# Kernel optimization log

Measured on AMD Instinct MI355X. Metric: run time of the kernel, lower is better.

The kernel has to match this reference:

```python
import jax, jax.numpy as jnp
import numpy as np
from jax import lax

EPS = 1e-4       # BatchNorm eps from module
THRESHOLD = 0.0  # TernaryActive threshold (default)

B, C_IN, H, W = 16, 32, 256, 256
C_OUT, K, STRIDE, PAD = 32, 3, 1, 1


def setup_inputs() -> dict:
    key = jax.random.key(0)
    ks = jax.random.split(key, 7)
    x = jax.random.normal(ks[0], (B, C_IN, H, W), dtype=jnp.float32)
    bn_gamma = jax.random.normal(ks[1], (C_IN,), dtype=jnp.float32) * 0.1 + 1.0
    bn_beta = jax.random.normal(ks[2], (C_IN,), dtype=jnp.float32) * 0.1
    bn_mean = jax.random.normal(ks[3], (C_IN,), dtype=jnp.float32) * 0.1
    bn_var = jax.random.uniform(ks[4], (C_IN,), dtype=jnp.float32, minval=0.5, maxval=1.5)
    fan_in = C_IN * K * K
    bound = 1.0 / np.sqrt(fan_in)
    conv_w = jax.random.uniform(ks[5], (C_OUT, C_IN, K, K), dtype=jnp.float32, minval=-bound, maxval=bound)
    conv_b = jax.random.uniform(ks[6], (C_OUT,), dtype=jnp.float32, minval=-bound, maxval=bound)
    return {"x": x, "bn_gamma": bn_gamma, "bn_beta": bn_beta,
            "bn_mean": bn_mean, "bn_var": bn_var,
            "conv_w": conv_w, "conv_b": conv_b}


def _ternary(x):
    # torch: output[x >= thr] = 1, then output[x <= -thr] = -1 (le overrides ge)
    return jnp.where(x <= -THRESHOLD, -1.0,
                     jnp.where(x >= THRESHOLD, 1.0, 0.0)).astype(x.dtype)


def reference(x, bn_gamma, bn_beta, bn_mean, bn_var, conv_w, conv_b):
    # BatchNorm2d (inference form with running stats), per-channel over C
    inv = bn_gamma / jnp.sqrt(bn_var + EPS)
    xh = x * inv[None, :, None, None] + (bn_beta - bn_mean * inv)[None, :, None, None]
    # Ternary quantize {-1, 0, 1}
    q = _ternary(xh)
    # Conv2d 3x3, stride 1, pad 1 (NCHW / OIHW)
    y = lax.conv_general_dilated(q, conv_w, window_strides=(STRIDE, STRIDE),
                                 padding=[(PAD, PAD), (PAD, PAD)],
                                 dimension_numbers=("NCHW", "OIHW", "NCHW"))
    y = y + conv_b[None, :, None, None]
    # ReLU
    return jnp.maximum(y, 0.0)
```

## Files before the change

kernel.cpp:

```cpp
#include <hip/hip_runtime.h>


#define B_    16
#define H_    256
#define W_    256
#define SW    32
#define YC    32
#define ROWB  2304
#define NITEM 576

typedef __bf16 bf16x8 __attribute__((ext_vector_type(8)));
typedef float  f32x4  __attribute__((ext_vector_type(4)));
union FragCast { int4 i; bf16x8 b; };

__device__ __forceinline__ unsigned short f2bf(float f) {
    union { float f; unsigned u; } c; c.f = f;
    unsigned u = c.u;
    u += 0x7FFFu + ((u >> 16) & 1u);
    return (unsigned short)(u >> 16);
}

__device__ __forceinline__ unsigned short quant1(float v, float sc, float sh) {
    float xh = __fadd_rn(__fmul_rn(v, sc), sh);
    return (xh <= 0.0f) ? (unsigned short)0xBF80u
         : ((xh >= 0.0f) ? (unsigned short)0x3F80u : (unsigned short)0u);
}

__launch_bounds__(256, 4)
__global__ void tbconv_kernel(const float* __restrict__ x,
                              const float* __restrict__ bn_g,
                              const float* __restrict__ bn_b,
                              const float* __restrict__ bn_m,
                              const float* __restrict__ bn_v,
                              const float* __restrict__ conv_w,
                              const float* __restrict__ conv_b,
                              float* __restrict__ out)
{
    __shared__ __align__(16) unsigned char smem[18432];
    __shared__ float sScale[32], sShift[32];
    unsigned int*  sW = (unsigned int*)smem;
    unsigned char* sQ = smem;

    const int tid = threadIdx.x;
    const int bx  = blockIdx.x;
    const int strip = bx >> 7;
    const int b     = (bx >> 3) & 15;
    const int yc    = bx & 7;
    const int x0 = strip * SW;
    const int y0 = yc * YC;

    if (tid < 32) {
        float s = __fdiv_rn(bn_g[tid], __fsqrt_rn(__fadd_rn(bn_v[tid], 1e-4f)));
        sScale[tid] = s;
        sShift[tid] = __fsub_rn(bn_b[tid], __fmul_rn(bn_m[tid], s));
    }
    for (int j = tid; j < 4608; j += 256) {
        int cp = j & 15, co = (j >> 4) & 31, t = j >> 9;
        float w0 = conv_w[(co * 32 + 2 * cp)     * 9 + t];
        float w1 = conv_w[(co * 32 + 2 * cp + 1) * 9 + t];
        sW[j] = (unsigned)f2bf(w0) | ((unsigned)f2bf(w1) << 16);
    }
    __syncthreads();

    const float* lp[3];
    int   lw0[3], lw1[3];
    float lsc[3], lsh[3];
    bool  lxok[3];
    const bool lv2 = (tid < 64);
    #pragma unroll
    for (int j = 0; j < 3; ++j) {
        int i = tid + 256 * j; if (i >= NITEM) i = 0;
        int ci = i / 18, pr = i - 18 * ci;
        int gx = x0 - 2 + 2 * pr;
        bool xok = (gx >= 0) && (gx < W_);
        int gxc = (gx < 0) ? 0 : ((gx > 254) ? 254 : gx);
        lp[j]   = x + (((size_t)(b * 32 + ci)) << 16) + gxc;
        lxok[j] = xok;
        int hx0 = 2 * pr - 1, hx1 = 2 * pr;
        int hc0 = (hx0 < 0)  ? 34 : hx0;
        int hc1 = (hx1 > 33) ? 35 : hx1;
        int q = ci >> 3, cl = ci & 7;
        lw0[j] = ((hc0 * 4 + (q ^ ((hc0 >> 1) & 3))) << 4) + cl * 2;
        lw1[j] = ((hc1 * 4 + (q ^ ((hc1 >> 1) & 3))) << 4) + cl * 2;
        lsc[j] = sScale[ci]; lsh[j] = sShift[ci];
    }

    const int lane = tid & 63, wave = tid >> 6;
    const int quad = lane >> 4, n = lane & 15;
    const int ct = wave >> 1, xh = wave & 1;
    const int xl = xh * 16 + n;

    FragCast fA[9];
    #pragma unroll
    for (int t = 0; t < 9; ++t)
        fA[t].i = *(const int4*)((const char*)sW + ((t * 32 + ct * 16 + n) * 32 + quad * 8) * 2);

    int dsoff[3];
    #pragma unroll
    for (int kw = 0; kw < 3; ++kw) {
        int hx = xl + kw;
        dsoff[kw] = (hx * 4 + (quad ^ ((hx >> 1) & 3))) << 4;
    }

    float bias[4];
    #pragma unroll
    for (int r = 0; r < 4; ++r)
        bias[r] = conv_b[ct * 16 + quad * 4 + r];
    const size_t obase = (((size_t)(b * 32 + ct * 16 + quad * 4)) << 16)
                       + ((size_t)y0 << 8) + (x0 + xl);

    __syncthreads();

    auto load_row = [&](float2 (&dv)[3], int gy) {
        bool yok = ((unsigned)gy < (unsigned)H_);
        #pragma unroll
        for (int j = 0; j < 3; ++j) {
            dv[j] = make_float2(0.f, 0.f);
            if (yok && (j < 2 || lv2))
                dv[j] = *(const float2*)(lp[j] + (gy << 8));
        }
    };
    auto scatter = [&](const float2 (&sv)[3], int gy, int slot) {
        bool yok = ((unsigned)gy < (unsigned)H_);
        char* rowp = (char*)sQ + slot * ROWB;
        #pragma unroll
        for (int j = 0; j < 3; ++j) {
            if (j < 2 || lv2) {
                unsigned short q0 = 0, q1 = 0;
                if (yok && lxok[j]) {
                    q0 = quant1(sv[j].x, lsc[j], lsh[j]);
                    q1 = quant1(sv[j].y, lsc[j], lsh[j]);
                }
                *(unsigned short*)(rowp + lw0[j]) = q0;
                *(unsigned short*)(rowp + lw1[j]) = q1;
            }
        }
    };

    float2 v[2][3];
    {
        float2 p0[3], p1[3], p2[3], p3[3];
        load_row(p0, y0 - 1); load_row(p1, y0);
        load_row(p2, y0 + 1); load_row(p3, y0 + 2);
        load_row(v[0], y0 + 3); load_row(v[1], y0 + 4);
        scatter(p0, y0 - 1, 7); scatter(p1, y0, 0);
        scatter(p2, y0 + 1, 1); scatter(p3, y0 + 2, 2);
    }
    __syncthreads();

    for (int t4 = 0; t4 < 4; ++t4) {
        #pragma unroll
        for (int u = 0; u < 4; ++u) {
            const int yy = t4 * 8 + u * 2;
            const int y  = y0 + yy;

            if (yy <= 28) {
                scatter(v[0], y + 3, (2 * u + 3) & 7);
                scatter(v[1], y + 4, (2 * u + 4) & 7);
            }
            __syncthreads();

            if (yy <= 26) {
                load_row(v[0], y + 5);
                load_row(v[1], y + 6);
            }

            f32x4 aA[3], aB[3];
            #pragma unroll
            for (int kh = 0; kh < 3; ++kh) {
                aA[kh] = (f32x4){0.f, 0.f, 0.f, 0.f};
                aB[kh] = (f32x4){0.f, 0.f, 0.f, 0.f};
            }
            #pragma unroll
            for (int j = 0; j < 4; ++j) {
                const int sb = ((2 * u + 7 + j) & 7) * ROWB;
                FragCast fB[3];
                #pragma unroll
                for (int kw = 0; kw < 3; ++kw)
                    fB[kw].i = *(const int4*)((const char*)sQ + sb + dsoff[kw]);
                #pragma unroll
                for (int kw = 0; kw < 3; ++kw) {
                    if (j < 3)
                        aA[j] = __builtin_amdgcn_mfma_f32_16x16x32_bf16(
                                    fA[j * 3 + kw].b, fB[kw].b, aA[j], 0, 0, 0);
                    if (j >= 1)
                        aB[j - 1] = __builtin_amdgcn_mfma_f32_16x16x32_bf16(
                                    fA[(j - 1) * 3 + kw].b, fB[kw].b, aB[j - 1], 0, 0, 0);
                }
            }

            #pragma unroll
            for (int r = 0; r < 4; ++r) {
                float sA = __fadd_rn(__fadd_rn(aA[0][r], aA[1][r]),
                                     __fadd_rn(aA[2][r], bias[r]));
                out[obase + ((size_t)r << 16) + ((size_t)yy << 8)] = fmaxf(sA, 0.f);
                float sB = __fadd_rn(__fadd_rn(aB[0][r], aB[1][r]),
                                     __fadd_rn(aB[2][r], bias[r]));
                out[obase + ((size_t)r << 16) + ((size_t)(yy + 1) << 8)] = fmaxf(sB, 0.f);
            }
        }
    }
}

extern "C" void kernel_launch(void* const* d_in, const int* in_sizes, int n_in,
                              void* d_out, int out_size, void* d_ws, size_t ws_size,
                              hipStream_t stream) {
    const float* x     = (const float*)d_in[0];
    const float* gamma = (const float*)d_in[1];
    const float* beta  = (const float*)d_in[2];
    const float* mean  = (const float*)d_in[3];
    const float* var   = (const float*)d_in[4];
    const float* w     = (const float*)d_in[5];
    const float* bias  = (const float*)d_in[6];
    float* o = (float*)d_out;

    dim3 grid(B_ * 8 * (H_ / YC));
    dim3 block(256);
    hipLaunchKernelGGL(tbconv_kernel, grid, block, 0, stream,
                       x, gamma, beta, mean, var, w, bias, o);
}
```

Baseline: 290.9 us.

## Deepen row pipeline with 16-slot LDS ring and lgkm-only barrier

The LDS ring of quantized rows grows from 8 to 16 slots, and global loads are issued one more row-pair ahead using two alternating register sets. This hides more global-memory latency behind the MFMA work. Each __syncthreads is replaced by an explicit lgkmcnt(0) wait plus s_barrier, so the barrier no longer waits on outstanding global loads. LDS use rises from 18 KB to 36 KB per block, which may cut occupancy below the 4 blocks per CU requested by launch bounds. Register pressure also grows.

```diff
diff --git a/kernel.cpp b/kernel.cpp
--- a/kernel.cpp
+++ b/kernel.cpp
@@ -24,6 +24,11 @@
     float xh = __fadd_rn(__fmul_rn(v, sc), sh);
     return (xh <= 0.0f) ? (unsigned short)0xBF80u
          : ((xh >= 0.0f) ? (unsigned short)0x3F80u : (unsigned short)0u);
+}
+
+__device__ __forceinline__ void lds_barrier() {
+    asm volatile("s_waitcnt lgkmcnt(0)" ::: "memory");
+    __builtin_amdgcn_s_barrier();
 }
 
 __launch_bounds__(256, 4)
@@ -36,7 +41,7 @@
                               const float* __restrict__ conv_b,
                               float* __restrict__ out)
 {
-    __shared__ __align__(16) unsigned char smem[18432];
+    __shared__ __align__(16) unsigned char smem[16 * ROWB];
     __shared__ float sScale[32], sShift[32];
     unsigned int*  sW = (unsigned int*)smem;
     unsigned char* sQ = smem;
@@ -137,33 +142,39 @@
         }
     };
 
-    float2 v[2][3];
+    float2 vE[2][3], vO[2][3];
     {
-        float2 p0[3], p1[3], p2[3], p3[3];
-        load_row(p0, y0 - 1); load_row(p1, y0);
-        load_row(p2, y0 + 1); load_row(p3, y0 + 2);
-        load_row(v[0], y0 + 3); load_row(v[1], y0 + 4);
-        scatter(p0, y0 - 1, 7); scatter(p1, y0, 0);
-        scatter(p2, y0 + 1, 1); scatter(p3, y0 + 2, 2);
-    }
-    __syncthreads();
-
-    for (int t4 = 0; t4 < 4; ++t4) {
+        float2 pA[2][3], pB[2][3];
+        load_row(pA[0], y0 - 1); load_row(pA[1], y0);
+        load_row(pB[0], y0 + 1); load_row(pB[1], y0 + 2);
+        scatter(pA[0], y0 - 1, 15); scatter(pA[1], y0, 0);
+        load_row(pA[0], y0 + 3); load_row(pA[1], y0 + 4);
+        scatter(pB[0], y0 + 1, 1); scatter(pB[1], y0 + 2, 2);
+        load_row(vE[0], y0 + 5); load_row(vE[1], y0 + 6);
+        scatter(pA[0], y0 + 3, 3); scatter(pA[1], y0 + 4, 4);
+    }
+    lds_barrier();
+
+    for (int t2 = 0; t2 < 2; ++t2) {
         #pragma unroll
-        for (int u = 0; u < 4; ++u) {
-            const int yy = t4 * 8 + u * 2;
-            const int y  = y0 + yy;
-
-            if (yy <= 28) {
-                scatter(v[0], y + 3, (2 * u + 3) & 7);
-                scatter(v[1], y + 4, (2 * u + 4) & 7);
-            }
-            __syncthreads();
-
-            if (yy <= 26) {
-                load_row(v[0], y + 5);
-                load_row(v[1], y + 6);
-            }
+        for (int u = 0; u < 8; ++u) {
+            const int k  = t2 * 8 + u;
+            const int y  = y0 + 2 * k;
+
+            if (k <= 12) {
+                if ((u & 1) == 0) { load_row(vO[0], y + 7); load_row(vO[1], y + 8); }
+                else              { load_row(vE[0], y + 7); load_row(vE[1], y + 8); }
+            }
+            if (k <= 13) {
+                if ((u & 1) == 0) {
+                    scatter(vE[0], y + 5, (2 * u + 5)  & 15);
+                    scatter(vE[1], y + 6, (2 * u + 6)  & 15);
+                } else {
+                    scatter(vO[0], y + 5, (2 * u + 5)  & 15);
+                    scatter(vO[1], y + 6, (2 * u + 6)  & 15);
+                }
+            }
+            lds_barrier();
 
             f32x4 aA[3], aB[3];
             #pragma unroll
@@ -173,7 +184,7 @@
             }
             #pragma unroll
             for (int j = 0; j < 4; ++j) {
-                const int sb = ((2 * u + 7 + j) & 7) * ROWB;
+                const int sb = ((2 * u + 15 + j) & 15) * ROWB;
                 FragCast fB[3];
                 #pragma unroll
                 for (int kw = 0; kw < 3; ++kw)
@@ -193,10 +204,10 @@
             for (int r = 0; r < 4; ++r) {
                 float sA = __fadd_rn(__fadd_rn(aA[0][r], aA[1][r]),
                                      __fadd_rn(aA[2][r], bias[r]));
-                out[obase + ((size_t)r << 16) + ((size_t)yy << 8)] = fmaxf(sA, 0.f);
+                out[obase + ((size_t)r << 16) + ((size_t)(2 * k) << 8)] = fmaxf(sA, 0.f);
                 float sB = __fadd_rn(__fadd_rn(aB[0][r], aB[1][r]),
                                      __fadd_rn(aB[2][r], bias[r]));
-                out[obase + ((size_t)r << 16) + ((size_t)(yy + 1) << 8)] = fmaxf(sB, 0.f);
+                out[obase + ((size_t)r << 16) + ((size_t)(2 * k + 1) << 8)] = fmaxf(sB, 0.f);
             }
         }
     }
```

Measured after the change: 284.1 us. 2.3% less time.
